# Optimization experiments

Measured on AMD Instinct MI355X. Metric: run time of the kernel, lower is better.

The kernel has to match this reference:

```python
import jax, jax.numpy as jnp
import numpy as np

PATCH_SIZE = 14
MERGE = 2  # spatial_merge_size
D = 1024
B = 8
IMG_PX = 1792  # 128 patches per side


def setup_inputs() -> dict:
    key = jax.random.key(0)
    k1, k2 = jax.random.split(key)
    n_patches_per_img = (IMG_PX // PATCH_SIZE) ** 2  # 16384
    total = B * n_patches_per_img                    # 131072
    image_features = jax.random.normal(k1, (1, total, D), dtype=jnp.float32)
    image_sizes = jnp.full((B, 2), IMG_PX, dtype=jnp.int32)
    # nn.Linear(D*MERGE**2, D, bias=False): weight (D, D*MERGE**2), y = x @ W.T
    W = jax.random.normal(k2, (D, D * MERGE * MERGE), dtype=jnp.float32) * (1.0 / np.sqrt(D * MERGE * MERGE))
    return {"image_features": image_features, "image_sizes": image_sizes, "W": W}


def _merge_one(xi, h, w, S):
    # xi: (h*w, D) in row-major (h, w) patch order
    d = xi.shape[-1]
    x = xi.reshape(h // S, S, w // S, S, d)
    # -> (h/S, w/S, D, S, S): matches torch unfold channel-major (d, ki, kj) column order
    x = x.transpose(0, 2, 4, 1, 3)
    return x.reshape((h // S) * (w // S), d * S * S)


def reference(image_features, image_sizes, W):
    sizes = np.asarray(image_sizes)  # static per-image pixel sizes
    x = image_features[0]  # (sum N_i, D)
    S = MERGE
    blocks = []
    off = 0
    for h_px, w_px in sizes:  # loop over B images (small, structurally distinct shapes)
        h, w = int(h_px) // PATCH_SIZE, int(w_px) // PATCH_SIZE
        n = h * w
        blocks.append(_merge_one(jax.lax.dynamic_slice_in_dim(x, off, n, axis=0), h, w, S))
        off += n
    merged = jnp.concatenate(blocks, axis=0)            # (sum L_i, D*S^2)
    out = jnp.einsum('nk,dk->nd', merged, W)            # single global GEMM
    return out[None, :, :]                              # (1, sum L_i, D)
```

## Files before the change

kernel.cpp:

```cpp
#include <hip/hip_runtime.h>
#include <hip/hip_bf16.h>
#include <stdint.h>


#define M_TOTAL 32768
#define K_DIM   4096
#define N_DIM   1024
#define BM 128
#define BN 128
#define BK 64

typedef __attribute__((ext_vector_type(8))) short short8;
typedef __attribute__((ext_vector_type(4))) float f32x4;
typedef __attribute__((ext_vector_type(8))) unsigned short us8;

#define ASYNC_COPY16(gsrc, ldst)                                                     \
    __builtin_amdgcn_global_load_lds(                                                \
        (const __attribute__((address_space(1))) unsigned int*)(const void*)(gsrc),  \
        (__attribute__((address_space(3))) unsigned int*)(ldst), 16, 0, 0)

static __device__ __forceinline__ unsigned pack2bf(float lo, float hi) {
    unsigned a = __builtin_bit_cast(unsigned, lo) + 0x8000u;
    unsigned b = __builtin_bit_cast(unsigned, hi) + 0x8000u;
    return __builtin_amdgcn_perm(b, a, 0x07060302);
}

__global__ __launch_bounds__(256) void repack_w(const float* __restrict__ W,
                                                unsigned short* __restrict__ Wp) {
    int t = blockIdx.x * 256 + threadIdx.x;
    int j  = t >> 8;
    int d0 = (t & 255) << 2;
    const float4* src = (const float4*)(W + (size_t)j * K_DIM + (size_t)d0 * 4);
    float4 v0 = src[0], v1 = src[1], v2 = src[2], v3 = src[3];
    float vs[4][4] = {{v0.x, v1.x, v2.x, v3.x},
                      {v0.y, v1.y, v2.y, v3.y},
                      {v0.z, v1.z, v2.z, v3.z},
                      {v0.w, v1.w, v2.w, v3.w}};
#pragma unroll
    for (int s = 0; s < 4; s++) {
        uint2 o;
        o.x = pack2bf(vs[s][0], vs[s][1]);
        o.y = pack2bf(vs[s][2], vs[s][3]);
        *(uint2*)(Wp + (size_t)j * K_DIM + s * 1024 + d0) = o;
    }
}

__global__ __launch_bounds__(256) void gather_convert(const float* __restrict__ X,
                                                      unsigned short* __restrict__ Ap) {
    int idx = blockIdx.x * 256 + threadIdx.x;
    int p   = idx >> 6;
    int c16 = (idx & 63) << 4;
    int img = p >> 14;
    int r   = p & 16383;
    int pi  = r >> 7;
    int pj  = r & 127;
    int m   = img * 4096 + (pi >> 1) * 64 + (pj >> 1);
    int s   = ((pi & 1) << 1) | (pj & 1);
    const float4* src = (const float4*)(X + (size_t)p * 1024 + c16);
    float4 v0 = src[0], v1 = src[1], v2 = src[2], v3 = src[3];
    uint4 o0, o1;
    o0.x = pack2bf(v0.x, v0.y); o0.y = pack2bf(v0.z, v0.w);
    o0.z = pack2bf(v1.x, v1.y); o0.w = pack2bf(v1.z, v1.w);
    o1.x = pack2bf(v2.x, v2.y); o1.y = pack2bf(v2.z, v2.w);
    o1.z = pack2bf(v3.x, v3.y); o1.w = pack2bf(v3.z, v3.w);
    uint4* dst = (uint4*)(Ap + (size_t)m * K_DIM + s * 1024 + c16);
    dst[0] = o0;
    dst[1] = o1;
}

__global__ __launch_bounds__(256) void gemm_bt(
        const unsigned short* __restrict__ Ap,
        const unsigned short* __restrict__ Wp,
        float* __restrict__ out) {
    __shared__ unsigned short As[BM * BK];
    __shared__ unsigned short Bs[BN * BK];

    const int tid  = threadIdx.x;
    const int lane = tid & 63;
    const int wave = tid >> 6;
    const int wm   = (wave >> 1) * 64;
    const int wn   = (wave & 1) * 64;
    const int lrow = lane & 15;
    const int quad = lane >> 4;

    const int blk = blockIdx.x;
    const int bn  = (blk & 7) * BN;
    const int bm  = (blk >> 3) * BM;

    const int rowoff = lane >> 3;
    const int cswz   = (lane & 7) ^ rowoff;
    const unsigned short* agp =
        Ap + (size_t)(bm + wave * 32 + rowoff) * K_DIM + cswz * 8;
    const unsigned short* bgp =
        Wp + (size_t)(bn + wave * 32 + rowoff) * K_DIM + cswz * 8;
    unsigned short* alp = As + (wave * 32) * BK;
    unsigned short* blp = Bs + (wave * 32) * BK;

    f32x4 acc[4][4] = {};

    for (int k0 = 0; k0 < K_DIM; k0 += BK) {
#pragma unroll
        for (int i = 0; i < 4; i++) {
            ASYNC_COPY16(agp + i * 8 * K_DIM + k0, alp + i * 8 * BK);
            ASYNC_COPY16(bgp + i * 8 * K_DIM + k0, blp + i * 8 * BK);
        }
        __syncthreads();

#pragma unroll
        for (int kk = 0; kk < 2; kk++) {
            const int c0 = kk * 4 + quad;
            short8 a[4], b[4];
#pragma unroll
            for (int i = 0; i < 4; i++) {
                const int ar = wm + i * 16 + lrow;
                a[i] = *(const short8*)&As[ar * BK + ((c0 ^ (lrow & 7)) << 3)];
            }
#pragma unroll
            for (int j = 0; j < 4; j++) {
                const int br = wn + j * 16 + lrow;
                b[j] = *(const short8*)&Bs[br * BK + ((c0 ^ (lrow & 7)) << 3)];
            }
#pragma unroll
            for (int i = 0; i < 4; i++)
#pragma unroll
                for (int j = 0; j < 4; j++)
                    acc[i][j] = __builtin_amdgcn_mfma_f32_16x16x32_bf16(
                        a[i], b[j], acc[i][j], 0, 0, 0);
        }
        __syncthreads();
    }

    const int ocol = bn + wn + lrow;
#pragma unroll
    for (int i = 0; i < 4; i++) {
#pragma unroll
        for (int r = 0; r < 4; r++) {
            float* po = out + (size_t)(bm + wm + i * 16 + quad * 4 + r) * N_DIM + ocol;
#pragma unroll
            for (int j = 0; j < 4; j++)
                po[j * 16] = acc[i][j][r];
        }
    }
}

#define LP 72
__global__ __launch_bounds__(256) void merge_gemm(
        const float* __restrict__ X,
        const unsigned short* __restrict__ Wp,
        float* __restrict__ out) {
    __shared__ unsigned short As[BM][LP];
    __shared__ unsigned short Bs[BN][LP];

    const int tid  = threadIdx.x;
    const int lane = tid & 63;
    const int wave = tid >> 6;
    const int wm   = (wave >> 1) * 64;
    const int wn   = (wave & 1) * 64;
    const int lrow = lane & 15;
    const int quad = lane >> 4;

    const int blk = blockIdx.x;
    const int bn  = (blk & 7) * BN;
    const int bm  = (blk >> 3) * BM;

    const int arow = tid >> 4;
    const int acol = (tid & 15) << 2;

    const float* abase[8];
#pragma unroll
    for (int rep = 0; rep < 8; rep++) {
        int m   = bm + arow + rep * 16;
        int img = m >> 12;
        int r   = m & 4095;
        int bi  = r >> 6;
        int bj  = r & 63;
        int pbase = img * 16384 + bi * 256 + bj * 2;
        abase[rep] = X + (size_t)pbase * 1024 + acol;
    }

    const int brow = tid >> 3;
    const int bcol = (tid & 7) << 3;

    f32x4 acc[4][4] = {};

    for (int k0 = 0; k0 < K_DIM; k0 += BK) {
        const int s    = k0 >> 10;
        const int d0   = k0 & 1023;
        const int aoff = (((s >> 1) * 128) + (s & 1)) * 1024 + d0;

#pragma unroll
        for (int rep = 0; rep < 8; rep++) {
            const float4 v = *(const float4*)(abase[rep] + aoff);
            uint2 o;
            o.x = pack2bf(v.x, v.y);
            o.y = pack2bf(v.z, v.w);
            *(uint2*)&As[arow + rep * 16][acol] = o;
        }
#pragma unroll
        for (int rep = 0; rep < 4; rep++) {
            us8 v = *(const us8*)(Wp + (size_t)(bn + brow + rep * 32) * K_DIM + k0 + bcol);
            *(us8*)&Bs[brow + rep * 32][bcol] = v;
        }
        __syncthreads();

#pragma unroll
        for (int kk = 0; kk < 2; kk++) {
            const int koff = kk * 32 + quad * 8;
            short8 a[4], b[4];
#pragma unroll
            for (int i = 0; i < 4; i++)
                a[i] = *(const short8*)&As[wm + i * 16 + lrow][koff];
#pragma unroll
            for (int j = 0; j < 4; j++)
                b[j] = *(const short8*)&Bs[wn + j * 16 + lrow][koff];
#pragma unroll
            for (int i = 0; i < 4; i++)
#pragma unroll
                for (int j = 0; j < 4; j++)
                    acc[i][j] = __builtin_amdgcn_mfma_f32_16x16x32_bf16(
                        a[i], b[j], acc[i][j], 0, 0, 0);
        }
        __syncthreads();
    }

    const int ocol = bn + wn + lrow;
#pragma unroll
    for (int i = 0; i < 4; i++) {
#pragma unroll
        for (int r = 0; r < 4; r++) {
            float* po = out + (size_t)(bm + wm + i * 16 + quad * 4 + r) * N_DIM + ocol;
#pragma unroll
            for (int j = 0; j < 4; j++)
                po[j * 16] = acc[i][j][r];
        }
    }
}

extern "C" void kernel_launch(void* const* d_in, const int* in_sizes, int n_in,
                              void* d_out, int out_size, void* d_ws, size_t ws_size,
                              hipStream_t stream) {
    const float* X = (const float*)d_in[0];
    const float* W = (const float*)d_in[2];
    float* out = (float*)d_out;

    unsigned short* Wp = (unsigned short*)d_ws;
    const size_t WP_BYTES = (size_t)N_DIM * K_DIM * 2;
    const size_t AP_BYTES = (size_t)M_TOTAL * K_DIM * 2;

    repack_w<<<dim3(1024), dim3(256), 0, stream>>>(W, Wp);

    if (ws_size >= WP_BYTES + AP_BYTES) {
        unsigned short* Ap = (unsigned short*)((char*)d_ws + WP_BYTES);
        gather_convert<<<dim3(32768), dim3(256), 0, stream>>>(X, Ap);
        gemm_bt<<<dim3((M_TOTAL / BM) * (N_DIM / BN)), dim3(256), 0, stream>>>(Ap, Wp, out);
    } else {
        merge_gemm<<<dim3((M_TOTAL / BM) * (N_DIM / BN)), dim3(256), 0, stream>>>(X, Wp, out);
    }
}
```

Baseline: 1.051 ms.

## Replace GEMM with 256x256-tile, 8-wave ping-pong pipelined MFMA kernel

Replaces the simple 128x128 single-buffered bf16 GEMM with a 256x256 tile kernel using 8 waves and double-buffered LDS. Global-to-LDS async copies are interleaved with the MFMA phases, paced by fine-grained barriers, explicit vmcnt/lgkmcnt waits and s_setprio. It also adds an XOR-swizzled LDS layout and an XCD-aware block remap. The aim is to hide memory latency behind compute and raise arithmetic intensity, at the cost of heavy register pressure and a fragile hand-scheduled synchronisation order.

```diff
diff --git a/kernel.cpp b/kernel.cpp
--- a/kernel.cpp
+++ b/kernel.cpp
@@ -68,74 +68,142 @@
     dst[1] = o1;
 }
 
-__global__ __launch_bounds__(256) void gemm_bt(
+#define NT 32
+
+#define SBAR() do { asm volatile("" ::: "memory");            \
+                    __builtin_amdgcn_s_barrier();             \
+                    asm volatile("" ::: "memory"); } while (0)
+#define WAITLG()  asm volatile("s_waitcnt lgkmcnt(0)" ::: "memory")
+#define WAITVM6() asm volatile("s_waitcnt vmcnt(6)" ::: "memory")
+
+__global__ __launch_bounds__(512, 2) void gemm_8p(
         const unsigned short* __restrict__ Ap,
         const unsigned short* __restrict__ Wp,
         float* __restrict__ out) {
-    __shared__ unsigned short As[BM * BK];
-    __shared__ unsigned short Bs[BN * BK];
+    __shared__ unsigned short lds[2][2][2][8192];
 
     const int tid  = threadIdx.x;
     const int lane = tid & 63;
     const int wave = tid >> 6;
-    const int wm   = (wave >> 1) * 64;
-    const int wn   = (wave & 1) * 64;
+    const int wr   = wave >> 2;
+    const int wc   = wave & 3;
     const int lrow = lane & 15;
     const int quad = lane >> 4;
 
-    const int blk = blockIdx.x;
-    const int bn  = (blk & 7) * BN;
-    const int bm  = (blk >> 3) * BM;
-
-    const int rowoff = lane >> 3;
-    const int cswz   = (lane & 7) ^ rowoff;
-    const unsigned short* agp =
-        Ap + (size_t)(bm + wave * 32 + rowoff) * K_DIM + cswz * 8;
-    const unsigned short* bgp =
-        Wp + (size_t)(bn + wave * 32 + rowoff) * K_DIM + cswz * 8;
-    unsigned short* alp = As + (wave * 32) * BK;
-    unsigned short* blp = Bs + (wave * 32) * BK;
-
-    f32x4 acc[4][4] = {};
-
-    for (int k0 = 0; k0 < K_DIM; k0 += BK) {
-#pragma unroll
-        for (int i = 0; i < 4; i++) {
-            ASYNC_COPY16(agp + i * 8 * K_DIM + k0, alp + i * 8 * BK);
-            ASYNC_COPY16(bgp + i * 8 * K_DIM + k0, blp + i * 8 * BK);
-        }
-        __syncthreads();
-
-#pragma unroll
-        for (int kk = 0; kk < 2; kk++) {
-            const int c0 = kk * 4 + quad;
-            short8 a[4], b[4];
-#pragma unroll
-            for (int i = 0; i < 4; i++) {
-                const int ar = wm + i * 16 + lrow;
-                a[i] = *(const short8*)&As[ar * BK + ((c0 ^ (lrow & 7)) << 3)];
-            }
-#pragma unroll
-            for (int j = 0; j < 4; j++) {
-                const int br = wn + j * 16 + lrow;
-                b[j] = *(const short8*)&Bs[br * BK + ((c0 ^ (lrow & 7)) << 3)];
-            }
-#pragma unroll
-            for (int i = 0; i < 4; i++)
-#pragma unroll
-                for (int j = 0; j < 4; j++)
-                    acc[i][j] = __builtin_amdgcn_mfma_f32_16x16x32_bf16(
-                        a[i], b[j], acc[i][j], 0, 0, 0);
-        }
-        __syncthreads();
-    }
-
-    const int ocol = bn + wn + lrow;
-#pragma unroll
-    for (int i = 0; i < 4; i++) {
+    const int bid = blockIdx.x;
+    const int lw  = (bid & 7) * 64 + (bid >> 3);
+    const int bn  = (lw & 3) * 256;
+    const int bm  = (lw >> 2) * 256;
+
+    const int rho   = lane >> 2;
+    const int kappa = (lane & 3) ^ ((lane >> 5) << 1);
+    const int r128s = wave * 16 + rho;
+    const unsigned short* aptr[2];
+    const unsigned short* bptr[2];
+#pragma unroll
+    for (int h = 0; h < 2; h++) {
+        const int ra = ((r128s >> 6) << 7) + h * 64 + (r128s & 63);
+        const int rb = ((r128s >> 5) << 6) + h * 32 + (r128s & 31);
+        aptr[h] = Ap + (size_t)(bm + ra) * K_DIM + kappa * 8;
+        bptr[h] = Wp + (size_t)(bn + rb) * K_DIM + kappa * 8;
+    }
+
+#define STAGE_A(slot, h, kt) do {                                                 \
+    ASYNC_COPY16(aptr[h] + (kt) * 64,      &lds[slot][0][h][wave * 1024]);        \
+    ASYNC_COPY16(aptr[h] + (kt) * 64 + 32, &lds[slot][0][h][wave * 1024 + 512]);  \
+} while (0)
+#define STAGE_B(slot, h, kt) do {                                                 \
+    ASYNC_COPY16(bptr[h] + (kt) * 64,      &lds[slot][1][h][wave * 1024]);        \
+    ASYNC_COPY16(bptr[h] + (kt) * 64 + 32, &lds[slot][1][h][wave * 1024 + 512]);  \
+} while (0)
+
+    const int rswz = (lrow * 64 + quad * 16) ^ ((lrow & 8) << 2);
+    short8 a[4][2], b0[2][2], b1[2][2];
+    f32x4 acc[8][4] = {};
+
+#define LDA(slot, mh) do {                                                        \
+    const char* base_ = (const char*)&lds[slot][0][mh][0] + rswz;                 \
+    _Pragma("unroll") for (int ii = 0; ii < 4; ii++)                              \
+    _Pragma("unroll") for (int kk = 0; kk < 2; kk++)                              \
+        a[ii][kk] = *(const short8*)(base_ + (wr * 4 + ii) * 2048 + kk * 1024);   \
+} while (0)
+#define LDB(slot, nh, breg) do {                                                  \
+    const char* base_ = (const char*)&lds[slot][1][nh][0] + rswz;                 \
+    _Pragma("unroll") for (int jj = 0; jj < 2; jj++)                              \
+    _Pragma("unroll") for (int kk = 0; kk < 2; kk++)                              \
+        breg[jj][kk] = *(const short8*)(base_ + (wc * 2 + jj) * 2048 + kk * 1024);\
+} while (0)
+#define MMA(mh, nh, breg) do {                                                    \
+    _Pragma("unroll") for (int ii = 0; ii < 4; ii++)                              \
+    _Pragma("unroll") for (int jj = 0; jj < 2; jj++)                              \
+    _Pragma("unroll") for (int kk = 0; kk < 2; kk++)                              \
+        acc[(mh) * 4 + ii][(nh) * 2 + jj] =                                       \
+            __builtin_amdgcn_mfma_f32_16x16x32_bf16(                              \
+                a[ii][kk], breg[jj][kk], acc[(mh) * 4 + ii][(nh) * 2 + jj],       \
+                0, 0, 0);                                                         \
+} while (0)
+
+    STAGE_B(0, 0, 0); STAGE_A(0, 0, 0); STAGE_B(0, 1, 0); STAGE_A(0, 1, 0);
+    STAGE_B(1, 0, 1); STAGE_A(1, 0, 1); STAGE_B(1, 1, 1);
+    WAITVM6();
+    SBAR();
+
+#pragma unroll 1
+    for (int t = 0; t < NT; t++) {
+        const int ko = 2 * t + 1;
+        const int ne = (2 * t + 2) & 63;
+        const int no = (2 * t + 3) & 63;
+
+        LDA(0, 0); LDB(0, 0, b0);
+        STAGE_A(1, 1, ko);
+        SBAR(); WAITLG();
+        __builtin_amdgcn_s_setprio(1); MMA(0, 0, b0); __builtin_amdgcn_s_setprio(0);
+        SBAR();
+        LDB(0, 1, b1);
+        STAGE_B(0, 0, ne);
+        SBAR(); WAITLG();
+        __builtin_amdgcn_s_setprio(1); MMA(0, 1, b1); __builtin_amdgcn_s_setprio(0);
+        SBAR();
+        LDA(0, 1);
+        STAGE_A(0, 0, ne);
+        SBAR(); WAITLG();
+        __builtin_amdgcn_s_setprio(1); MMA(1, 0, b0); __builtin_amdgcn_s_setprio(0);
+        SBAR();
+        STAGE_B(0, 1, ne);
+        SBAR();
+        __builtin_amdgcn_s_setprio(1); MMA(1, 1, b1); __builtin_amdgcn_s_setprio(0);
+        WAITVM6();
+        SBAR();
+        LDA(1, 0); LDB(1, 0, b0);
+        STAGE_A(0, 1, ne);
+        SBAR(); WAITLG();
+        __builtin_amdgcn_s_setprio(1); MMA(0, 0, b0); __builtin_amdgcn_s_setprio(0);
+        SBAR();
+        LDB(1, 1, b1);
+        STAGE_B(1, 0, no);
+        SBAR(); WAITLG();
+        __builtin_amdgcn_s_setprio(1); MMA(0, 1, b1); __builtin_amdgcn_s_setprio(0);
+        SBAR();
+        LDA(1, 1);
+        STAGE_A(1, 0, no);
+        SBAR(); WAITLG();
+        __builtin_amdgcn_s_setprio(1); MMA(1, 0, b0); __builtin_amdgcn_s_setprio(0);
+        SBAR();
+        STAGE_B(1, 1, no);
+        SBAR();
+        __builtin_amdgcn_s_setprio(1); MMA(1, 1, b1); __builtin_amdgcn_s_setprio(0);
+        WAITVM6();
+        SBAR();
+    }
+
+    asm volatile("s_waitcnt vmcnt(0)" ::: "memory");
+
+    const int ocol = bn + wc * 64 + lrow;
+#pragma unroll
+    for (int i = 0; i < 8; i++) {
 #pragma unroll
         for (int r = 0; r < 4; r++) {
-            float* po = out + (size_t)(bm + wm + i * 16 + quad * 4 + r) * N_DIM + ocol;
+            float* po = out + (size_t)(bm + wr * 128 + i * 16 + quad * 4 + r) * N_DIM + ocol;
 #pragma unroll
             for (int j = 0; j < 4; j++)
                 po[j * 16] = acc[i][j][r];
@@ -252,7 +320,7 @@
     if (ws_size >= WP_BYTES + AP_BYTES) {
         unsigned short* Ap = (unsigned short*)((char*)d_ws + WP_BYTES);
         gather_convert<<<dim3(32768), dim3(256), 0, stream>>>(X, Ap);
-        gemm_bt<<<dim3((M_TOTAL / BM) * (N_DIM / BN)), dim3(256), 0, stream>>>(Ap, Wp, out);
+        gemm_8p<<<dim3(512), dim3(512), 0, stream>>>(Ap, Wp, out);
     } else {
         merge_gemm<<<dim3((M_TOTAL / BM) * (N_DIM / BN)), dim3(256), 0, stream>>>(X, Wp, out);
     }
```

Result: faster. 964.9 us (-8.2%).
